# Kernel tuning notes

Hardware: AMD Instinct MI355X
Metric: run time of the kernel (lower is better)

Reference implementation:

```python
import jax, jax.numpy as jnp
import numpy as np

B, N = 32, 200000          # images, flattened candidates per image (anchors*classes)
NUM_CLASSES = 21           # VOC-style class count for the label-offset trick
CONF_THR = 0.05            # cfg.PRED_CONF_THR
NMS_THR = 0.5              # cfg.PRED_NMS_THR
TOPK = 500                 # cfg.PRED_SELECT_TOPK
KEEP_MAX = 100             # cfg.PRED_NMS_KEEP


def setup_inputs() -> dict:
    key = jax.random.key(0)
    k1, k2, k3, k4 = jax.random.split(key, 4)
    pscores = jax.random.uniform(k1, (B, N), dtype=jnp.float32)
    # well-formed ltrb boxes in [0,1]: right>left, bottom>top
    xy1 = jax.random.uniform(k2, (B, N, 2), dtype=jnp.float32) * 0.8
    wh = jax.random.uniform(k3, (B, N, 2), dtype=jnp.float32) * 0.2 + 0.01
    pboxes = jnp.concatenate([xy1, xy1 + wh], axis=-1)
    plabels = jax.random.randint(k4, (B, N), 0, NUM_CLASSES)
    return {"pscores": pscores, "pboxes": pboxes, "plabels": plabels}


def _box_iou(a, b):
    # a: [K,4], b: [K,4] ltrb -> [K,K] pairwise IoU (torchvision convention)
    lt = jnp.maximum(a[:, None, :2], b[None, :, :2])
    rb = jnp.minimum(a[:, None, 2:], b[None, :, 2:])
    wh = jnp.clip(rb - lt, 0.0)
    inter = wh[..., 0] * wh[..., 1]
    area_a = (a[:, 2] - a[:, 0]) * (a[:, 3] - a[:, 1])
    area_b = (b[:, 2] - b[:, 0]) * (b[:, 3] - b[:, 1])
    return inter / (area_a[:, None] + area_b[None, :] - inter)


def _greedy_nms(iou_mat, valid, thr):
    # candidates are pre-sorted by score descending (lax.top_k output order)
    K = valid.shape[0]
    idxs = jnp.arange(K)

    def body(keep, i):
        suppressed = jnp.any(keep & (iou_mat[i] > thr) & (idxs < i))
        k = valid[i] & (~suppressed)
        return keep.at[i].set(k), None

    keep, _ = jax.lax.scan(body, jnp.zeros((K,), dtype=bool), idxs)
    return keep


def reference(pscores, pboxes, plabels):
    # ---- threshold + top-k pre-selection (mask_pos AND mask_topk) ----
    scores_k, idx = jax.lax.top_k(pscores, TOPK)          # [B,K] sorted desc
    valid = scores_k > CONF_THR                           # equivalent to mask_pos & mask_topk
    bidx = jnp.arange(B)[:, None]
    boxes_k = pboxes[bidx, idx]                           # [B,K,4]
    labels_k = plabels[bidx, idx]                         # [B,K]

    # ---- multi-class NMS via label offset trick (batched_nms) ----
    max_coord = jnp.max(jnp.where(valid[..., None], boxes_k, 0.0), axis=(1, 2))  # [B]
    offsets = labels_k.astype(boxes_k.dtype) * (max_coord[:, None] + 1.0)
    boxes_nms = boxes_k + offsets[..., None]              # [B,K,4]

    iou = jax.vmap(_box_iou)(boxes_nms, boxes_nms)        # [B,K,K]
    keep = jax.vmap(lambda m, v: _greedy_nms(m, v, NMS_THR))(iou, valid)  # [B,K] bool

    # ---- keep[:num_max] per batch ----
    rank = jnp.cumsum(keep.astype(jnp.int32), axis=1)
    keep = keep & (rank <= KEEP_MAX)

    # compact kept entries to front (jnp.argsort is stable -> score order preserved), pad to KEEP_MAX
    order = jnp.argsort(jnp.where(keep, 0, 1), axis=1)[:, :KEEP_MAX]       # [B,KEEP]
    out_valid = jnp.take_along_axis(keep, order, axis=1)                    # [B,KEEP]
    boxes2 = jnp.take_along_axis(boxes_k, order[..., None], axis=1) * out_valid[..., None]
    scores2 = jnp.take_along_axis(scores_k, order, axis=1) * out_valid
    labels2 = jnp.where(out_valid, jnp.take_along_axis(labels_k, order, axis=1), -1)
    ids_batch2 = jnp.where(out_valid, jnp.arange(B)[:, None], -1)
    return ids_batch2, boxes2, labels2, scores2, out_valid
```

## Files before the change

kernel.cpp:

```cpp
#include <hip/hip_runtime.h>
#include <stdint.h>

#pragma clang fp contract(off)

#define BB 32
#define NN 200000
#define N4 50000
#define KK 500
#define KEEPN 100
#define CONF 0.05f
#define NMSTHR 0.5f
#define SLICES 8
#define SLICE_F4 6250
#define LBINS 8192
#define LSHIFT 19
#define LOCAL_CAP 2048
#define OUT_CAP 576
#define M_CAP (SLICES * OUT_CAP)
#define OK0 0xBF733333u

typedef unsigned long long u64;


__device__ __forceinline__ unsigned int ordkey(float s) {
    unsigned int u = __float_as_uint(s);
    return (u & 0x80000000u) ? ~u : (u | 0x80000000u);
}

__device__ __forceinline__ void wappend(bool pred, u64 key, u64* keys, int* lcnt, int lane) {
    u64 bm = __ballot(pred);
    int pre = __popcll(bm & ((1ULL << lane) - 1ULL));
    int tt  = __popcll(bm);
    int base = 0;
    if (lane == 0 && tt > 0) base = atomicAdd(lcnt, tt);
    base = __shfl(base, 0);
    if (pred) { int pos = base + pre; if (pos < LOCAL_CAP) keys[pos] = key; }
}

__global__ __launch_bounds__(1024) void select_kernel(const float4* __restrict__ ps4,
                                                      u64* __restrict__ cand,
                                                      unsigned int* __restrict__ cnts) {
    __shared__ unsigned int hist[LBINS];
    __shared__ u64 keys[LOCAL_CAP];
    __shared__ unsigned int h[256];
    __shared__ unsigned int wsum[16];
    __shared__ u64 s_prefix;
    __shared__ unsigned int s_t13, s_region, s_cntgt;
    __shared__ int s_lcnt, s_sc;

    const int b = blockIdx.y, x = blockIdx.x;
    const int tid = threadIdx.x, lane = tid & 63, wv = tid >> 6;
    const float4* p = ps4 + (size_t)b * N4 + (size_t)x * SLICE_F4;
    const int ebase = x * (SLICE_F4 * 4);

    if (tid == 0) s_lcnt = 0;
    __syncthreads();

    for (int i = tid; i < SLICE_F4; i += 1024) {
        float4 v = p[i];
        int n = ebase + (i << 2);
        unsigned int ux = ordkey(v.x), uy = ordkey(v.y);
        unsigned int uz = ordkey(v.z), uw = ordkey(v.w);
        wappend(ux >= OK0, ((u64)ux << 32) | (unsigned int)(~(unsigned int)(n)),     keys, &s_lcnt, lane);
        wappend(uy >= OK0, ((u64)uy << 32) | (unsigned int)(~(unsigned int)(n + 1)), keys, &s_lcnt, lane);
        wappend(uz >= OK0, ((u64)uz << 32) | (unsigned int)(~(unsigned int)(n + 2)), keys, &s_lcnt, lane);
        wappend(uw >= OK0, ((u64)uw << 32) | (unsigned int)(~(unsigned int)(n + 3)), keys, &s_lcnt, lane);
    }
    __syncthreads();
    int m = s_lcnt;

    if (m < KK || m > LOCAL_CAP) {
        for (int i = tid; i < LBINS; i += 1024) hist[i] = 0;
        __syncthreads();
        for (int i = tid; i < SLICE_F4; i += 1024) {
            float4 v = p[i];
            atomicAdd(&hist[ordkey(v.x) >> LSHIFT], 1u);
            atomicAdd(&hist[ordkey(v.y) >> LSHIFT], 1u);
            atomicAdd(&hist[ordkey(v.z) >> LSHIFT], 1u);
            atomicAdd(&hist[ordkey(v.w) >> LSHIFT], 1u);
        }
        __syncthreads();
        unsigned int v8[8], tot = 0;
        for (int j = 0; j < 8; ++j) { v8[j] = hist[tid * 8 + j]; tot += v8[j]; }
        unsigned int sfx = tot;
        for (int off = 1; off < 64; off <<= 1) {
            unsigned int t2 = __shfl_down(sfx, off);
            sfx += (lane + off < 64) ? t2 : 0u;
        }
        if (lane == 0) wsum[wv] = sfx;
        __syncthreads();
        unsigned int wafter = 0;
        for (int w2 = wv + 1; w2 < 16; ++w2) wafter += wsum[w2];
        unsigned int sn = wafter + (sfx - tot);
        for (int j = 7; j >= 0; --j) {
            unsigned int s = sn + v8[j];
            if (s >= (unsigned)KK && sn < (unsigned)KK) s_t13 = (unsigned)(tid * 8 + j);
            sn = s;
        }
        if (tid == 0) s_lcnt = 0;
        __syncthreads();
        const unsigned int t13 = s_t13;
        for (int i = tid; i < SLICE_F4; i += 1024) {
            float4 v = p[i];
            int n = ebase + (i << 2);
            unsigned int u;
            u = ordkey(v.x); if ((u >> LSHIFT) >= t13) { int pos = atomicAdd(&s_lcnt, 1);
                if (pos < LOCAL_CAP) keys[pos] = ((u64)u << 32) | (unsigned int)(~(unsigned int)(n)); }
            u = ordkey(v.y); if ((u >> LSHIFT) >= t13) { int pos = atomicAdd(&s_lcnt, 1);
                if (pos < LOCAL_CAP) keys[pos] = ((u64)u << 32) | (unsigned int)(~(unsigned int)(n + 1)); }
            u = ordkey(v.z); if ((u >> LSHIFT) >= t13) { int pos = atomicAdd(&s_lcnt, 1);
                if (pos < LOCAL_CAP) keys[pos] = ((u64)u << 32) | (unsigned int)(~(unsigned int)(n + 2)); }
            u = ordkey(v.w); if ((u >> LSHIFT) >= t13) { int pos = atomicAdd(&s_lcnt, 1);
                if (pos < LOCAL_CAP) keys[pos] = ((u64)u << 32) | (unsigned int)(~(unsigned int)(n + 3)); }
        }
        __syncthreads();
        m = s_lcnt; if (m > LOCAL_CAP) m = LOCAL_CAP;
    }

    u64 thr; int seln;
    if (m <= OUT_CAP) {
        thr = 0ULL; seln = m;
    } else {
        if (tid == 0) { s_prefix = 0ULL; s_cntgt = 0u; }
        __syncthreads();
        int shift = 56;
        for (; shift >= 0; shift -= 8) {
            if (tid < 256) h[tid] = 0u;
            __syncthreads();
            u64 pref = s_prefix;
            unsigned int cg = s_cntgt;
            for (int i = tid; i < m; i += 1024) {
                u64 k = keys[i];
                bool match = (shift == 56) || ((k >> (shift + 8)) == pref);
                if (match) atomicAdd(&h[(unsigned int)((k >> shift) & 0xFF)], 1u);
            }
            __syncthreads();
            if (wv == 0) {
                unsigned int b4[4]; unsigned int lt = 0;
                for (int j = 0; j < 4; ++j) { b4[j] = h[lane * 4 + j]; lt += b4[j]; }
                unsigned int sx = lt;
                for (int off = 1; off < 64; off <<= 1) {
                    unsigned int t2 = __shfl_down(sx, off);
                    sx += (lane + off < 64) ? t2 : 0u;
                }
                unsigned int after = sx - lt;
                unsigned int target = (unsigned)KK - cg;
                unsigned int sn2 = after;
                for (int j = 3; j >= 0; --j) {
                    unsigned int s = sn2 + b4[j];
                    if (s >= target && sn2 < target) {
                        unsigned int bin = (unsigned)(lane * 4 + j);
                        s_region = b4[j];
                        s_cntgt = cg + sn2;
                        s_prefix = (shift == 56) ? (u64)bin : ((pref << 8) | (u64)bin);
                    }
                    sn2 = s;
                }
            }
            __syncthreads();
            if (s_cntgt + s_region <= (unsigned)OUT_CAP) break;
        }
        if (shift < 0) shift = 0;
        thr = s_prefix << shift;
        seln = (int)(s_cntgt + s_region);
    }
    (void)seln;

    if (tid == 0) s_sc = 0;
    __syncthreads();
    u64* outslice = cand + (size_t)(b * SLICES + x) * OUT_CAP;
    for (int r0 = 0; r0 < LOCAL_CAP / 1024; ++r0) {
        int i = tid + r0 * 1024;
        u64 k = (i < m) ? keys[i] : 0ULL;
        bool pq = (i < m) && (k >= thr);
        u64 mb = __ballot(pq);
        int pre = __popcll(mb & ((1ULL << lane) - 1ULL));
        int tt = __popcll(mb);
        int base = 0;
        if (lane == 0 && tt > 0) base = atomicAdd(&s_sc, tt);
        base = __shfl(base, 0);
        if (pq && base + pre < OUT_CAP) outslice[base + pre] = k;
    }
    __syncthreads();
    if (tid == 0) {
        int c = s_sc; if (c > OUT_CAP) c = OUT_CAP;
        cnts[b * SLICES + x] = (unsigned)c;
    }
}

__global__ __launch_bounds__(1024) void final_kernel(const float* __restrict__ pboxes,
                                                     const int* __restrict__ plabels,
                                                     const u64* __restrict__ cand,
                                                     const unsigned int* __restrict__ cnts,
                                                     float* __restrict__ out) {
    __shared__ u64 kbuf[M_CAP];
    __shared__ u64 sel[OUT_CAP];
    __shared__ float sboxes[KK * 4];
    __shared__ float sscore[KK];
    __shared__ int slabel[KK];
    __shared__ int clist[KK];
    __shared__ unsigned int h[256];
    __shared__ int ccnt[21], coff[22], cfill[21];
    __shared__ u64 validw[8];
    __shared__ u64 sremv[8];
    __shared__ u64 s_km;
    __shared__ int kept[KEEPN];
    __shared__ float wred[16];
    __shared__ int soff[SLICES + 1];
    __shared__ u64 s_prefix;
    __shared__ unsigned int s_region, s_cntgt;
    __shared__ int s_sc, s_nk, s_stop;
    __shared__ float s_maxc;

    const int b = blockIdx.x;
    const int tid = threadIdx.x;
    const int lane = tid & 63;
    const int wv = tid >> 6;

    if (tid == 0) {
        int acc = 0;
        for (int s = 0; s < SLICES; ++s) {
            soff[s] = acc;
            int c = (int)cnts[b * SLICES + s];
            if (c > OUT_CAP) c = OUT_CAP;
            acc += c;
        }
        soff[SLICES] = acc;
    }
    __syncthreads();
    int m = soff[SLICES];
    for (int s = 0; s < SLICES; ++s) {
        int off = soff[s], len = soff[s + 1] - off;
        const u64* src = cand + (size_t)(b * SLICES + s) * OUT_CAP;
        for (int i = tid; i < len; i += 1024) kbuf[off + i] = src[i];
    }
    __syncthreads();

    u64 thr; int seln;
    if (m <= OUT_CAP) {
        thr = 0ULL; seln = m;
    } else {
        if (tid == 0) { s_prefix = 0ULL; s_cntgt = 0u; }
        __syncthreads();
        int shift = 56;
        for (; shift >= 0; shift -= 8) {
            if (tid < 256) h[tid] = 0u;
            __syncthreads();
            u64 pref = s_prefix;
            unsigned int cg = s_cntgt;
            for (int i = tid; i < m; i += 1024) {
                u64 k = kbuf[i];
                bool match = (shift == 56) || ((k >> (shift + 8)) == pref);
                if (match) atomicAdd(&h[(unsigned int)((k >> shift) & 0xFF)], 1u);
            }
            __syncthreads();
            if (wv == 0) {
                unsigned int b4[4]; unsigned int lt = 0;
                for (int j = 0; j < 4; ++j) { b4[j] = h[lane * 4 + j]; lt += b4[j]; }
                unsigned int sx = lt;
                for (int off = 1; off < 64; off <<= 1) {
                    unsigned int t2 = __shfl_down(sx, off);
                    sx += (lane + off < 64) ? t2 : 0u;
                }
                unsigned int after = sx - lt;
                unsigned int target = (unsigned)KK - cg;
                unsigned int sn2 = after;
                for (int j = 3; j >= 0; --j) {
                    unsigned int s = sn2 + b4[j];
                    if (s >= target && sn2 < target) {
                        unsigned int bin = (unsigned)(lane * 4 + j);
                        s_region = b4[j];
                        s_cntgt = cg + sn2;
                        s_prefix = (shift == 56) ? (u64)bin : ((pref << 8) | (u64)bin);
                    }
                    sn2 = s;
                }
            }
            __syncthreads();
            if (s_cntgt + s_region <= (unsigned)OUT_CAP) break;
        }
        if (shift < 0) shift = 0;
        thr = s_prefix << shift;
        seln = (int)(s_cntgt + s_region);
    }

    if (tid == 0) s_sc = 0;
    __syncthreads();
    for (int r0 = 0; r0 < (M_CAP + 1023) / 1024; ++r0) {
        int i = tid + r0 * 1024;
        u64 k = (i < m) ? kbuf[i] : 0ULL;
        bool pq = (i < m) && (k >= thr);
        u64 mb = __ballot(pq);
        int pre = __popcll(mb & ((1ULL << lane) - 1ULL));
        int tt = __popcll(mb);
        int base = 0;
        if (lane == 0 && tt > 0) base = atomicAdd(&s_sc, tt);
        base = __shfl(base, 0);
        if (pq) sel[base + pre] = k;
    }
    __syncthreads();

    u64 myk = (tid < seln) ? sel[tid] : 0ULL;
    int r = 0;
    if ((tid & ~63) < seln) {
        for (int base = 0; base < seln; base += 64) {
            int i2 = base + lane;
            u64 other = (i2 < seln) ? sel[i2] : 0ULL;
            unsigned int olo = (unsigned int)other, ohi = (unsigned int)(other >> 32);
            int lim = seln - base; if (lim > 64) lim = 64;
            for (int t2 = 0; t2 < lim; ++t2) {
                unsigned int blo = (unsigned int)__builtin_amdgcn_readlane((int)olo, t2);
                unsigned int bhi = (unsigned int)__builtin_amdgcn_readlane((int)ohi, t2);
                u64 o = ((u64)bhi << 32) | (u64)blo;
                r += (o > myk) ? 1 : 0;
            }
        }
    }
    __syncthreads();
    if (tid < seln && r < KK) sel[r] = myk;
    __syncthreads();

    float sc = -1.0f;
    if (tid < KK) {
        u64 key = sel[tid];
        unsigned int lo = (unsigned int)key;
        unsigned int hi = (unsigned int)(key >> 32);
        int idx = (int)(~lo);
        unsigned int bits = (hi & 0x80000000u) ? (hi & 0x7FFFFFFFu) : ~hi;
        sc = __uint_as_float(bits);
        sscore[tid] = sc;
        const float4 bx = *(const float4*)(pboxes + (((size_t)b * NN + (size_t)idx) << 2));
        sboxes[tid * 4 + 0] = bx.x; sboxes[tid * 4 + 1] = bx.y;
        sboxes[tid * 4 + 2] = bx.z; sboxes[tid * 4 + 3] = bx.w;
        slabel[tid] = plabels[(size_t)b * NN + idx];
    }
    __syncthreads();

    bool vq = (tid < KK) && (sc > CONF);
    u64 bm = __ballot(vq);
    if (lane == 0 && wv < 8) validw[wv] = bm;
    float lm = vq ? fmaxf(fmaxf(sboxes[tid * 4 + 0], sboxes[tid * 4 + 1]),
                          fmaxf(sboxes[tid * 4 + 2], sboxes[tid * 4 + 3])) : 0.0f;
    for (int off = 32; off > 0; off >>= 1) lm = fmaxf(lm, __shfl_down(lm, off));
    if (lane == 0) wred[wv] = lm;
    __syncthreads();
    if (tid < 64) {
        float x = (tid < 16) ? wred[tid] : 0.0f;
        for (int off = 8; off > 0; off >>= 1) x = fmaxf(x, __shfl_down(x, off));
        if (tid == 0) s_maxc = x;
    }
    if (tid < 21) { ccnt[tid] = 0; cfill[tid] = 0; }
    if (tid < 8) sremv[tid] = 0ULL;
    if (tid == 0) { s_nk = 0; s_stop = 0; }
    __syncthreads();
    if (tid < KK) atomicAdd(&ccnt[slabel[tid]], 1);
    __syncthreads();
    if (tid == 0) {
        int acc = 0;
        for (int c = 0; c < 21; ++c) { coff[c] = acc; acc += ccnt[c]; }
        coff[21] = acc;
    }
    __syncthreads();
    if (tid < KK) {
        int c = slabel[tid];
        int pos = atomicAdd(&cfill[c], 1);
        clist[coff[c] + pos] = tid;
    }
    u64 (*msk)[512] = (u64(*)[512])kbuf;
    for (int i = tid; i < 8 * 512; i += 1024) ((u64*)kbuf)[i] = 0ULL;
    __syncthreads();

    float ap1 = s_maxc + 1.0f;
    if (tid < KK) {
        int c = slabel[tid];
        int n = ccnt[c], base0 = coff[c];
        float aoff = (float)c * ap1;
        float a0 = sboxes[tid * 4 + 0] + aoff, a1 = sboxes[tid * 4 + 1] + aoff;
        float a2 = sboxes[tid * 4 + 2] + aoff, a3 = sboxes[tid * 4 + 3] + aoff;
        float areaA = (a2 - a0) * (a3 - a1);
        for (int q = 0; q < n; ++q) {
            int j = clist[base0 + q];
            float b0 = sboxes[j * 4 + 0] + aoff, b1f = sboxes[j * 4 + 1] + aoff;
            float b2f = sboxes[j * 4 + 2] + aoff, b3f = sboxes[j * 4 + 3] + aoff;
            float lt0 = fmaxf(a0, b0), lt1 = fmaxf(a1, b1f);
            float rb0 = fminf(a2, b2f), rb1 = fminf(a3, b3f);
            float ww = fmaxf(rb0 - lt0, 0.0f), hh = fmaxf(rb1 - lt1, 0.0f);
            float inter = ww * hh;
            float areaB = (b2f - b0) * (b3f - b1f);
            float iou = inter / (areaA + areaB - inter);
            if (iou > NMSTHR) msk[j >> 6][tid] |= (1ULL << (j & 63));
        }
    }
    __syncthreads();

    for (int c = 0; c < 8; ++c) {
        if (wv == 0) {
            u64 rowc = msk[c][c * 64 + lane];
            unsigned int rl = (unsigned int)rowc, rh = (unsigned int)(rowc >> 32);
            u64 cur = sremv[c];
            u64 vv = validw[c];
            u64 km = 0ULL;
            int nk = s_nk;
            for (int j = 0; j < 64; ++j) {
                if (nk >= KEEPN) break;
                bool alive = (((vv >> j) & 1ULL) != 0ULL) && (((cur >> j) & 1ULL) == 0ULL);
                if (alive) {
                    if (lane == 0) kept[nk] = c * 64 + j;
                    u64 rv = ((u64)(unsigned int)__builtin_amdgcn_readlane((int)rh, j) << 32)
                           |  (u64)(unsigned int)__builtin_amdgcn_readlane((int)rl, j);
                    cur |= rv;
                    km |= (1ULL << j);
                    ++nk;
                }
            }
            if (lane == 0) { s_km = km; s_nk = nk; sremv[c] = cur; s_stop = (nk >= KEEPN) ? 1 : 0; }
        }
        __syncthreads();
        if (s_stop || c == 7) break;
        if (wv > c && wv < 8) {
            u64 km = s_km;
            u64 v = ((km >> lane) & 1ULL) ? msk[wv][c * 64 + lane] : 0ULL;
            for (int off2 = 32; off2 > 0; off2 >>= 1) v |= __shfl_xor(v, off2);
            if (lane == 0) sremv[wv] |= v;
        }
        __syncthreads();
    }

    if (tid < KEEPN) {
        const int O_BOX = BB * KEEPN;
        const int O_LAB = BB * KEEPN * 5;
        const int O_SCO = BB * KEEPN * 6;
        const int O_VAL = BB * KEEPN * 7;
        bool q = tid < s_nk;
        int i = q ? kept[tid] : 0;
        int g = b * KEEPN + tid;
        out[g]                 = q ? (float)b : -1.0f;
        out[O_BOX + g * 4 + 0] = q ? sboxes[i * 4 + 0] : 0.0f;
        out[O_BOX + g * 4 + 1] = q ? sboxes[i * 4 + 1] : 0.0f;
        out[O_BOX + g * 4 + 2] = q ? sboxes[i * 4 + 2] : 0.0f;
        out[O_BOX + g * 4 + 3] = q ? sboxes[i * 4 + 3] : 0.0f;
        out[O_LAB + g]         = q ? (float)slabel[i] : -1.0f;
        out[O_SCO + g]         = q ? sscore[i] : 0.0f;
        out[O_VAL + g]         = q ? 1.0f : 0.0f;
    }
}

extern "C" void kernel_launch(void* const* d_in, const int* in_sizes, int n_in,
                              void* d_out, int out_size, void* d_ws, size_t ws_size,
                              hipStream_t stream) {
    const float* pscores = (const float*)d_in[0];
    const float* pboxes  = (const float*)d_in[1];
    const int*   plabels = (const int*)d_in[2];
    float* out = (float*)d_out;

    uint8_t* ws = (uint8_t*)d_ws;
    u64*          cand = (u64*)(ws + 0);
    unsigned int* cnts = (unsigned int*)(ws + 1179648);

    select_kernel<<<dim3(SLICES, BB), 1024, 0, stream>>>((const float4*)pscores, cand, cnts);
    final_kernel<<<BB, 1024, 0, stream>>>(pboxes, plabels, cand, cnts, out);
}
```

Baseline: 227.6 us.

## Skip redundant radix-select passes via min/max prefix, prefetch boxes before rank scatter

Before the byte-wise radix select in both kernels, a block-wide min/max of the candidate keys fixes the common high-byte prefix, so the histogram passes start at the first differing byte. In the final kernel, each thread loads its candidate's box and label from global memory before the rank computation and scatters them straight to the ranked slot, which removes a shared round-trip and a barrier and lets the gather latency overlap the ranking. The box array stride changes from 4 to 5 floats, likely to reduce LDS bank conflicts in the IoU loop. Slice counts are loaded in parallel instead of serially by one thread. The cost is an extra reduction pass and barrier, plus box and label loads for up to OUT_CAP candidates rather than only the top KK.

```diff
diff --git a/kernel.cpp b/kernel.cpp
--- a/kernel.cpp
+++ b/kernel.cpp
@@ -44,9 +44,10 @@
     __shared__ u64 keys[LOCAL_CAP];
     __shared__ unsigned int h[256];
     __shared__ unsigned int wsum[16];
+    __shared__ u64 wmin[16], wmax[16];
     __shared__ u64 s_prefix;
     __shared__ unsigned int s_t13, s_region, s_cntgt;
-    __shared__ int s_lcnt, s_sc;
+    __shared__ int s_lcnt, s_sc, s_shift0;
 
     const int b = blockIdx.y, x = blockIdx.x;
     const int tid = threadIdx.x, lane = tid & 63, wv = tid >> 6;
@@ -121,9 +122,32 @@
     if (m <= OUT_CAP) {
         thr = 0ULL; seln = m;
     } else {
-        if (tid == 0) { s_prefix = 0ULL; s_cntgt = 0u; }
-        __syncthreads();
-        int shift = 56;
+        u64 kmn = ~0ULL, kmx = 0ULL;
+        for (int i = tid; i < m; i += 1024) {
+            u64 k = keys[i];
+            kmn = k < kmn ? k : kmn; kmx = k > kmx ? k : kmx;
+        }
+        for (int off = 32; off > 0; off >>= 1) {
+            u64 a = __shfl_down(kmn, off), c = __shfl_down(kmx, off);
+            if (lane + off < 64) { kmn = a < kmn ? a : kmn; kmx = c > kmx ? c : kmx; }
+        }
+        if (lane == 0) { wmin[wv] = kmn; wmax[wv] = kmx; }
+        __syncthreads();
+        if (tid == 0) {
+            u64 mn = wmin[0], mx = wmax[0];
+            for (int w2 = 1; w2 < 16; ++w2) {
+                mn = wmin[w2] < mn ? wmin[w2] : mn;
+                mx = wmax[w2] > mx ? wmax[w2] : mx;
+            }
+            u64 diff = mn ^ mx;
+            int hb = 63 - __builtin_clzll(diff | 1ULL);
+            int st = (hb >> 3) << 3;
+            s_shift0 = st;
+            s_prefix = (st == 56) ? 0ULL : (mx >> (st + 8));
+            s_cntgt = 0u;
+        }
+        __syncthreads();
+        int shift = s_shift0;
         for (; shift >= 0; shift -= 8) {
             if (tid < 256) h[tid] = 0u;
             __syncthreads();
@@ -195,21 +219,23 @@
                                                      float* __restrict__ out) {
     __shared__ u64 kbuf[M_CAP];
     __shared__ u64 sel[OUT_CAP];
-    __shared__ float sboxes[KK * 4];
+    __shared__ float sboxes[KK * 5];
     __shared__ float sscore[KK];
     __shared__ int slabel[KK];
     __shared__ int clist[KK];
     __shared__ unsigned int h[256];
     __shared__ int ccnt[21], coff[22], cfill[21];
+    __shared__ int scnt[SLICES];
     __shared__ u64 validw[8];
     __shared__ u64 sremv[8];
     __shared__ u64 s_km;
     __shared__ int kept[KEEPN];
     __shared__ float wred[16];
+    __shared__ u64 wmin[16], wmax[16];
     __shared__ int soff[SLICES + 1];
     __shared__ u64 s_prefix;
     __shared__ unsigned int s_region, s_cntgt;
-    __shared__ int s_sc, s_nk, s_stop;
+    __shared__ int s_sc, s_nk, s_stop, s_shift0;
     __shared__ float s_maxc;
 
     const int b = blockIdx.x;
@@ -217,14 +243,15 @@
     const int lane = tid & 63;
     const int wv = tid >> 6;
 
+    if (tid < SLICES) {
+        int c = (int)cnts[b * SLICES + tid];
+        if (c > OUT_CAP) c = OUT_CAP;
+        scnt[tid] = c;
+    }
+    __syncthreads();
     if (tid == 0) {
         int acc = 0;
-        for (int s = 0; s < SLICES; ++s) {
-            soff[s] = acc;
-            int c = (int)cnts[b * SLICES + s];
-            if (c > OUT_CAP) c = OUT_CAP;
-            acc += c;
-        }
+        for (int s = 0; s < SLICES; ++s) { soff[s] = acc; acc += scnt[s]; }
         soff[SLICES] = acc;
     }
     __syncthreads();
@@ -240,9 +267,32 @@
     if (m <= OUT_CAP) {
         thr = 0ULL; seln = m;
     } else {
-        if (tid == 0) { s_prefix = 0ULL; s_cntgt = 0u; }
-        __syncthreads();
-        int shift = 56;
+        u64 kmn = ~0ULL, kmx = 0ULL;
+        for (int i = tid; i < m; i += 1024) {
+            u64 k = kbuf[i];
+            kmn = k < kmn ? k : kmn; kmx = k > kmx ? k : kmx;
+        }
+        for (int off = 32; off > 0; off >>= 1) {
+            u64 a = __shfl_down(kmn, off), c = __shfl_down(kmx, off);
+            if (lane + off < 64) { kmn = a < kmn ? a : kmn; kmx = c > kmx ? c : kmx; }
+        }
+        if (lane == 0) { wmin[wv] = kmn; wmax[wv] = kmx; }
+        __syncthreads();
+        if (tid == 0) {
+            u64 mn = wmin[0], mx = wmax[0];
+            for (int w2 = 1; w2 < 16; ++w2) {
+                mn = wmin[w2] < mn ? wmin[w2] : mn;
+                mx = wmax[w2] > mx ? wmax[w2] : mx;
+            }
+            u64 diff = mn ^ mx;
+            int hb = 63 - __builtin_clzll(diff | 1ULL);
+            int st = (hb >> 3) << 3;
+            s_shift0 = st;
+            s_prefix = (st == 56) ? 0ULL : (mx >> (st + 8));
+            s_cntgt = 0u;
+        }
+        __syncthreads();
+        int shift = s_shift0;
         for (; shift >= 0; shift -= 8) {
             if (tid < 256) h[tid] = 0u;
             __syncthreads();
@@ -301,6 +351,23 @@
     __syncthreads();
 
     u64 myk = (tid < seln) ? sel[tid] : 0ULL;
+    float mysc = -1.0f; int mylab = 0;
+    float4 mybx = make_float4(0.0f, 0.0f, 0.0f, 0.0f);
+    if (tid < seln) {
+        unsigned int lo = (unsigned int)myk;
+        unsigned int hi = (unsigned int)(myk >> 32);
+        int idx = (int)(~lo);
+        unsigned int bits = (hi & 0x80000000u) ? (hi & 0x7FFFFFFFu) : ~hi;
+        mysc = __uint_as_float(bits);
+        mybx = *(const float4*)(pboxes + (((size_t)b * NN + (size_t)idx) << 2));
+        mylab = plabels[(size_t)b * NN + idx];
+    }
+    if (tid < KK) {
+        sscore[tid] = -1.0f; slabel[tid] = 0;
+        sboxes[tid * 5 + 0] = 0.0f; sboxes[tid * 5 + 1] = 0.0f;
+        sboxes[tid * 5 + 2] = 0.0f; sboxes[tid * 5 + 3] = 0.0f;
+    }
+
     int r = 0;
     if ((tid & ~63) < seln) {
         for (int base = 0; base < seln; base += 64) {
@@ -317,30 +384,19 @@
         }
     }
     __syncthreads();
-    if (tid < seln && r < KK) sel[r] = myk;
-    __syncthreads();
-
-    float sc = -1.0f;
-    if (tid < KK) {
-        u64 key = sel[tid];
-        unsigned int lo = (unsigned int)key;
-        unsigned int hi = (unsigned int)(key >> 32);
-        int idx = (int)(~lo);
-        unsigned int bits = (hi & 0x80000000u) ? (hi & 0x7FFFFFFFu) : ~hi;
-        sc = __uint_as_float(bits);
-        sscore[tid] = sc;
-        const float4 bx = *(const float4*)(pboxes + (((size_t)b * NN + (size_t)idx) << 2));
-        sboxes[tid * 4 + 0] = bx.x; sboxes[tid * 4 + 1] = bx.y;
-        sboxes[tid * 4 + 2] = bx.z; sboxes[tid * 4 + 3] = bx.w;
-        slabel[tid] = plabels[(size_t)b * NN + idx];
-    }
-    __syncthreads();
-
+    if (tid < seln && r < KK) {
+        sboxes[r * 5 + 0] = mybx.x; sboxes[r * 5 + 1] = mybx.y;
+        sboxes[r * 5 + 2] = mybx.z; sboxes[r * 5 + 3] = mybx.w;
+        sscore[r] = mysc; slabel[r] = mylab;
+    }
+    __syncthreads();
+
+    float sc = (tid < KK) ? sscore[tid] : -1.0f;
     bool vq = (tid < KK) && (sc > CONF);
     u64 bm = __ballot(vq);
     if (lane == 0 && wv < 8) validw[wv] = bm;
-    float lm = vq ? fmaxf(fmaxf(sboxes[tid * 4 + 0], sboxes[tid * 4 + 1]),
-                          fmaxf(sboxes[tid * 4 + 2], sboxes[tid * 4 + 3])) : 0.0f;
+    float lm = vq ? fmaxf(fmaxf(sboxes[tid * 5 + 0], sboxes[tid * 5 + 1]),
+                          fmaxf(sboxes[tid * 5 + 2], sboxes[tid * 5 + 3])) : 0.0f;
     for (int off = 32; off > 0; off >>= 1) lm = fmaxf(lm, __shfl_down(lm, off));
     if (lane == 0) wred[wv] = lm;
     __syncthreads();
@@ -375,13 +431,13 @@
         int c = slabel[tid];
         int n = ccnt[c], base0 = coff[c];
         float aoff = (float)c * ap1;
-        float a0 = sboxes[tid * 4 + 0] + aoff, a1 = sboxes[tid * 4 + 1] + aoff;
-        float a2 = sboxes[tid * 4 + 2] + aoff, a3 = sboxes[tid * 4 + 3] + aoff;
+        float a0 = sboxes[tid * 5 + 0] + aoff, a1 = sboxes[tid * 5 + 1] + aoff;
+        float a2 = sboxes[tid * 5 + 2] + aoff, a3 = sboxes[tid * 5 + 3] + aoff;
         float areaA = (a2 - a0) * (a3 - a1);
         for (int q = 0; q < n; ++q) {
             int j = clist[base0 + q];
-            float b0 = sboxes[j * 4 + 0] + aoff, b1f = sboxes[j * 4 + 1] + aoff;
-            float b2f = sboxes[j * 4 + 2] + aoff, b3f = sboxes[j * 4 + 3] + aoff;
+            float b0 = sboxes[j * 5 + 0] + aoff, b1f = sboxes[j * 5 + 1] + aoff;
+            float b2f = sboxes[j * 5 + 2] + aoff, b3f = sboxes[j * 5 + 3] + aoff;
             float lt0 = fmaxf(a0, b0), lt1 = fmaxf(a1, b1f);
             float rb0 = fminf(a2, b2f), rb1 = fminf(a3, b3f);
             float ww = fmaxf(rb0 - lt0, 0.0f), hh = fmaxf(rb1 - lt1, 0.0f);
@@ -435,10 +491,10 @@
         int i = q ? kept[tid] : 0;
         int g = b * KEEPN + tid;
         out[g]                 = q ? (float)b : -1.0f;
-        out[O_BOX + g * 4 + 0] = q ? sboxes[i * 4 + 0] : 0.0f;
-        out[O_BOX + g * 4 + 1] = q ? sboxes[i * 4 + 1] : 0.0f;
-        out[O_BOX + g * 4 + 2] = q ? sboxes[i * 4 + 2] : 0.0f;
-        out[O_BOX + g * 4 + 3] = q ? sboxes[i * 4 + 3] : 0.0f;
+        out[O_BOX + g * 4 + 0] = q ? sboxes[i * 5 + 0] : 0.0f;
+        out[O_BOX + g * 4 + 1] = q ? sboxes[i * 5 + 1] : 0.0f;
+        out[O_BOX + g * 4 + 2] = q ? sboxes[i * 5 + 2] : 0.0f;
+        out[O_BOX + g * 4 + 3] = q ? sboxes[i * 5 + 3] : 0.0f;
         out[O_LAB + g]         = q ? (float)slabel[i] : -1.0f;
         out[O_SCO + g]         = q ? sscore[i] : 0.0f;
         out[O_VAL + g]         = q ? 1.0f : 0.0f;
```

Result: faster. 218.6 us (-4.0%).
